# Optimization experiments

Measured on AMD Instinct MI355X. Metric: run time of the kernel, lower is better.

Reference implementation:

```python
import jax, jax.numpy as jnp
import numpy as np

B, T, D = 2, 2048, 2048
H, HD = 16, 128
HHD = HD // 2
SCALE = 1.0 / np.sqrt(HHD).astype(np.float32)


def setup_inputs() -> dict:
    key = jax.random.key(0)
    ks = jax.random.split(key, 6)
    s = 1.0 / np.sqrt(D).astype(np.float32)
    return {
        "x": jax.random.normal(ks[0], (B, T, D), jnp.float32),
        "Wq": jax.random.normal(ks[1], (D, H * HD), jnp.float32) * s,
        "Wk": jax.random.normal(ks[2], (D, H * HD), jnp.float32) * s,
        "Wv": jax.random.normal(ks[3], (D, H * HD), jnp.float32) * s,
        "Wo": jax.random.normal(ks[4], (H * HD, D), jnp.float32) * s,
        "lambda_init": jnp.full((H,), -0.2, jnp.float32),
    }


def reference(x, Wq, Wk, Wv, Wo, lambda_init):
    b, t, d = x.shape
    # projections -> (B, H, T, HD)
    q = (x @ Wq).reshape(b, t, H, HD).transpose(0, 2, 1, 3)
    k = (x @ Wk).reshape(b, t, H, HD).transpose(0, 2, 1, 3)
    v = (x @ Wv).reshape(b, t, H, HD).transpose(0, 2, 1, 3)
    q1, q2 = q[..., :HHD], q[..., HHD:]
    k1, k2 = k[..., :HHD], k[..., HHD:]
    scores1 = jnp.einsum('bhtc,bhsc->bhts', q1, k1) * SCALE
    scores2 = jnp.einsum('bhtc,bhsc->bhts', q2, k2) * SCALE
    causal = jnp.tril(jnp.ones((t, t), bool))  # (T, T)
    neg_inf = jnp.float32(-jnp.inf)
    scores1 = jnp.where(causal[None, None], scores1, neg_inf)
    scores2 = jnp.where(causal[None, None], scores2, neg_inf)
    attn1 = jax.nn.softmax(scores1, axis=-1)
    attn2 = jax.nn.softmax(scores2, axis=-1)
    lam = jax.nn.sigmoid(lambda_init)[None, :, None, None]
    diff_attn = attn1 - lam * attn2
    out = jnp.einsum('bhts,bhsd->bhtd', diff_attn, v)
    out = out.transpose(0, 2, 1, 3).reshape(b, t, H * HD)
    return out @ Wo
```

## Files before the change

kernel.cpp:

```cpp
#include <hip/hip_runtime.h>
#include <cstdint>
#include <cstddef>


typedef unsigned short u16;
typedef __bf16 bf16x8 __attribute__((ext_vector_type(8)));
typedef float f32x4 __attribute__((ext_vector_type(4)));

#define LOG2E 1.44269504088896340736f
#define KS 0.18033688011112042f
#define CB 11.541560327111707f

__device__ __forceinline__ u16 f2bu(float f) {
  unsigned int x = __float_as_uint(f);
  x += 0x7fffu + ((x >> 16) & 1u);
  return (u16)(x >> 16);
}

__device__ __forceinline__ void stage16(const void* g, void* lds_uniform, int lane) {
#if defined(__has_builtin) && __has_builtin(__builtin_amdgcn_global_load_lds)
  (void)lane;
  __builtin_amdgcn_global_load_lds(
      (__attribute__((address_space(1))) void*)(g),
      (__attribute__((address_space(3))) void*)(lds_uniform), 16, 0, 0);
#else
  *(uint4*)((char*)lds_uniform + lane * 16) = *(const uint4*)g;
#endif
}

__global__ void f32_to_bf16_k(const float* __restrict__ in, u16* __restrict__ out, int n4) {
  int i = blockIdx.x * blockDim.x + threadIdx.x;
  if (i < n4) {
    float4 v = ((const float4*)in)[i];
    ushort4 u;
    u.x = f2bu(v.x); u.y = f2bu(v.y); u.z = f2bu(v.z); u.w = f2bu(v.w);
    ((ushort4*)out)[i] = u;
  }
}

__global__ void transpose_f32_bf16(const float* __restrict__ in, u16* __restrict__ out,
                                   int R, int C) {
  __shared__ u16 tile[32][33];
  const int tx = threadIdx.x & 31, ty = threadIdx.x >> 5;
  const int c0 = blockIdx.x * 32, r0 = blockIdx.y * 32;
#pragma unroll
  for (int i = 0; i < 32; i += 8)
    tile[ty + i][tx] = f2bu(in[(size_t)(r0 + ty + i) * C + c0 + tx]);
  __syncthreads();
#pragma unroll
  for (int i = 0; i < 32; i += 8)
    out[(size_t)(c0 + ty + i) * R + r0 + tx] = tile[tx][ty + i];
}

template <int MODE>
__global__ void gemm_bt(const u16* __restrict__ A, const u16* __restrict__ BT,
                        void* __restrict__ C, u16* __restrict__ C2,
                        int Mdim, int Ndim, int Kdim) {
  __shared__ __align__(16) u16 As[128 * 32];
  __shared__ __align__(16) u16 Bs[128 * 32];
  const int tid = threadIdx.x;
  const int lane = tid & 63;
  const int w = tid >> 6;
  const int wm = w & 1, wn = w >> 1;
  const int li = lane & 15, lh = lane >> 4;
  const int m0 = blockIdx.x * 128;
  const int n0 = blockIdx.y * 128;

  const f32x4 fzero = {0.f, 0.f, 0.f, 0.f};
  f32x4 acc[4][4];
#pragma unroll
  for (int i = 0; i < 4; ++i)
#pragma unroll
    for (int jj = 0; jj < 4; ++jj) acc[i][jj] = fzero;

  for (int k0 = 0; k0 < Kdim; k0 += 32) {
#pragma unroll
    for (int i = 0; i < 2; ++i) {
      const int c = i * 256 + w * 64 + lane;
      stage16(A + (size_t)(m0 + (c >> 2)) * Kdim + k0 + ((c & 3) << 3),
              (char*)As + (size_t)(i * 256 + w * 64) * 16, lane);
      stage16(BT + (size_t)(n0 + (c >> 2)) * Kdim + k0 + ((c & 3) << 3),
              (char*)Bs + (size_t)(i * 256 + w * 64) * 16, lane);
    }
    __syncthreads();

    bf16x8 af[4], bfr[4];
#pragma unroll
    for (int mt = 0; mt < 4; ++mt)
      af[mt] = *(const bf16x8*)&As[(wm * 64 + mt * 16 + li) * 32 + lh * 8];
#pragma unroll
    for (int nt = 0; nt < 4; ++nt)
      bfr[nt] = *(const bf16x8*)&Bs[(wn * 64 + nt * 16 + li) * 32 + lh * 8];
#pragma unroll
    for (int mt = 0; mt < 4; ++mt)
#pragma unroll
      for (int nt = 0; nt < 4; ++nt)
        acc[mt][nt] = __builtin_amdgcn_mfma_f32_16x16x32_bf16(af[mt], bfr[nt], acc[mt][nt], 0, 0, 0);
    __syncthreads();
  }

#pragma unroll
  for (int mt = 0; mt < 4; ++mt) {
#pragma unroll
    for (int nt = 0; nt < 4; ++nt) {
      const int mb = m0 + wm * 64 + mt * 16 + lh * 4;
      const int n = n0 + wn * 64 + nt * 16 + li;
      if (MODE == 0) {
        u16* o = (u16*)C;
#pragma unroll
        for (int r = 0; r < 4; ++r)
          o[(size_t)(mb + r) * Ndim + n] = f2bu(acc[mt][nt][r]);
      } else if (MODE == 1) {
        float* o = (float*)C;
#pragma unroll
        for (int r = 0; r < 4; ++r)
          o[(size_t)(mb + r) * Ndim + n] = acc[mt][nt][r];
      } else {
        u16* o = (u16*)C;
        const int bb = mb >> 11, t = mb & 2047;
        const int hh = n >> 7, d = n & 127;
        ushort4 u;
        u.x = f2bu(acc[mt][nt][0]);
        u.y = f2bu(acc[mt][nt][1]);
        u.z = f2bu(acc[mt][nt][2]);
        u.w = f2bu(acc[mt][nt][3]);
        *(ushort4*)&o[((size_t)((bb * 16 + hh) * 128 + d) << 11) + t] = u;
      }
    }
  }
}

__device__ __forceinline__ void stage_half256(const u16* __restrict__ gbase, int Kdim,
                                              u16* lds_slot, int tid) {
#pragma unroll
  for (int j = 0; j < 2; ++j) {
    const int c = j * 512 + tid;
    const int ks = c >> 9;
    const int o = (c & 511) << 4;
    const int osz = o ^ (((o >> 9) & 1) << 5);
    const int row = osz >> 6;
    const int kel = (osz & 63) >> 1;
    stage16(gbase + (size_t)row * Kdim + ks * 32 + kel,
            (char*)lds_slot + ((size_t)(j * 512 + (tid & ~63)) << 4), tid & 63);
  }
}

#define PHASE256(MH, KS, LOADB, STAGESTMT, TAILSTMT)                           \
  {                                                                            \
    bf16x8 af[4];                                                              \
    _Pragma("unroll")                                                          \
    for (int mq = 0; mq < 4; ++mq)                                             \
      af[mq] = *(const bf16x8*)&As[sA][KS][((MH)*4 + mq) * 16 + li][lhx8];     \
    if (LOADB) {                                                               \
      _Pragma("unroll")                                                        \
      for (int nt = 0; nt < 4; ++nt)                                           \
        bfc[nt] = *(const bf16x8*)&Bs[sB][KS][brow + nt * 16 + li][lhx8];      \
    }                                                                          \
    STAGESTMT;                                                                 \
    __builtin_amdgcn_s_barrier();                                              \
    asm volatile("" ::: "memory");                                             \
    __builtin_amdgcn_s_setprio(1);                                             \
    _Pragma("unroll")                                                          \
    for (int mq = 0; mq < 4; ++mq) {                                           \
      _Pragma("unroll")                                                        \
      for (int nt = 0; nt < 4; ++nt)                                           \
        acc[(MH)*4 + mq][nt] = __builtin_amdgcn_mfma_f32_16x16x32_bf16(        \
            af[mq], bfc[nt], acc[(MH)*4 + mq][nt], 0, 0, 0);                   \
    }                                                                          \
    __builtin_amdgcn_s_setprio(0);                                             \
    TAILSTMT;                                                                  \
    __builtin_amdgcn_s_barrier();                                              \
    asm volatile("" ::: "memory");                                             \
  }

__global__ __launch_bounds__(512, 2)
void gemm256_qkv(const u16* __restrict__ A, const u16* __restrict__ BT,
                 u16* __restrict__ C, u16* __restrict__ C2, int Kdim) {
  __shared__ __align__(16) u16 As[5][2][128][32];
  __shared__ __align__(16) u16 Bs[4][2][128][32];

  const int tid = threadIdx.x;
  const int lane = tid & 63;
  const int w = tid >> 6;
  const int wm = w >> 2;
  const int wn = w & 3;
  const int li = lane & 15, lh = lane >> 4;
  const int lhx8 = (lh ^ (((li >> 3) & 1) << 1)) * 8;
  const int brow = (wn & 1) * 64;

  const int bid = blockIdx.x;
  const int xcd = bid & 7;
  const int local = bid >> 3;
  const int mtile = local / 3;
  const int ntile = xcd * 3 + (local % 3);
  const int m0 = mtile * 256, n0 = ntile * 256;

  const int NT = Kdim >> 6;
  const u16* Abase = A + (size_t)m0 * Kdim;
  const u16* Bbase = BT + (size_t)n0 * Kdim;

  auto stA = [&](int g) {
    if (g < 2 * NT)
      stage_half256(Abase + (size_t)((g & 1) * 128) * Kdim + (g >> 1) * 64, Kdim,
                    &As[g % 5][0][0][0], tid);
  };
  auto stB = [&](int g) {
    if (g < 2 * NT)
      stage_half256(Bbase + (size_t)((g & 1) * 128) * Kdim + (g >> 1) * 64, Kdim,
                    &Bs[g & 3][0][0][0], tid);
  };

  const f32x4 fzero = {0.f, 0.f, 0.f, 0.f};
  f32x4 acc[8][4];
#pragma unroll
  for (int i = 0; i < 8; ++i)
#pragma unroll
    for (int jj = 0; jj < 4; ++jj) acc[i][jj] = fzero;

  stA(0); stA(1); stB(0); stB(1); stA(2); stB(2); stB(3);
  asm volatile("s_waitcnt vmcnt(6)" ::: "memory");
  __builtin_amdgcn_s_barrier();
  asm volatile("" ::: "memory");

  bf16x8 bfc[4];
  for (int kt = 0; kt < NT; ++kt) {
    const int sA = (2 * kt + wm) % 5;
    const int sB = (2 * kt + (wn >> 1)) & 3;
    PHASE256(0, 0, 1, { stA(2 * kt + 3); stA(2 * kt + 4); }, ((void)0));
    PHASE256(1, 0, 0, ((void)0), ((void)0));
    PHASE256(0, 1, 1, ((void)0), ((void)0));
    PHASE256(1, 1, 0, { stB(2 * kt + 4); stB(2 * kt + 5); },
             if (kt + 2 < NT) { asm volatile("s_waitcnt vmcnt(6)" ::: "memory"); }
             else             { asm volatile("s_waitcnt vmcnt(0)" ::: "memory"); });
  }

  const int proj = n0 >> 11;
  const int nB = (n0 & 2047) + wn * 64;
  const int mB = m0 + wm * 128;
#pragma unroll
  for (int mt = 0; mt < 8; ++mt) {
#pragma unroll
    for (int nt = 0; nt < 4; ++nt) {
      const int mb = mB + mt * 16 + lh * 4;
      const int n = nB + nt * 16 + li;
      if (proj < 2) {
        u16* o = C + (size_t)proj * 4096 * 2048;
#pragma unroll
        for (int r = 0; r < 4; ++r)
          o[(size_t)(mb + r) * 2048 + n] = f2bu(acc[mt][nt][r]);
      } else {
        const int bb = mb >> 11, t = mb & 2047;
        const int hh = n >> 7, d = n & 127;
        ushort4 u;
        u.x = f2bu(acc[mt][nt][0]);
        u.y = f2bu(acc[mt][nt][1]);
        u.z = f2bu(acc[mt][nt][2]);
        u.w = f2bu(acc[mt][nt][3]);
        *(ushort4*)&C2[((size_t)((bb * 16 + hh) * 128 + d) << 11) + t] = u;
      }
    }
  }
}

__device__ __forceinline__ void stage_kv(const u16* __restrict__ kbase,
                                         const u16* __restrict__ vbase, int j,
                                         u16* ksBuf, u16* vsBuf, int w, int lane) {
  const int kst_r = lane >> 4, kst_c = lane & 15;
  const int vst_r = lane >> 3, vst_c = lane & 7;
#pragma unroll
  for (int i = 0; i < 4; ++i) {
    const int t = w * 4 + i;
    const int srow = t * 4 + kst_r;
    const int scb = kst_c ^ (srow & 7);
    stage16(kbase + (size_t)(j * 64 + srow) * 2048 + scb * 8,
            (char*)ksBuf + t * 1024, lane);
    const int drow = t * 8 + vst_r;
    const int dcb = vst_c ^ (drow & 7);
    stage16(vbase + (size_t)drow * 2048 + j * 64 + dcb * 8,
            (char*)vsBuf + t * 1024, lane);
  }
}

__global__ __launch_bounds__(256, 2)
void diff_attn(const u16* __restrict__ Q, const u16* __restrict__ K,
               const u16* __restrict__ VT, const float* __restrict__ lamin,
               u16* __restrict__ AO) {
  __shared__ __align__(16) u16 Ks[2][64 * 128];
  __shared__ __align__(16) u16 Vs[2][128 * 64];
  __shared__ __align__(16) u16 Ps1[64 * 64];
  __shared__ __align__(16) u16 Ps2[64 * 64];

  const int tid = threadIdx.x, lane = tid & 63, w = tid >> 6;
  const int li = lane & 15, lh = lane >> 4;
  const int bh = blockIdx.x & 31, pair = blockIdx.x >> 5;
  const int b = bh >> 4, h = bh & 15;

  const float lam = 1.f / (1.f + exp2f(-lamin[h] * LOG2E));
  const u16* kbase = K + ((size_t)(b * 2048)) * 2048 + h * 128;
  const u16* vbase = VT + ((size_t)(b * 16 + h) << 18);
  const f32x4 fzero = {0.f, 0.f, 0.f, 0.f};

  for (int phase = 0; phase < 2; ++phase) {
    const int it = phase ? 31 - pair : pair;
    const int t0 = it * 64;

    bf16x8 qf[4];
    {
      const u16* qp = Q + (size_t)(b * 2048 + t0 + w * 16 + li) * 2048 + h * 128 + lh * 8;
#pragma unroll
      for (int kk = 0; kk < 4; ++kk) qf[kk] = *(const bf16x8*)(qp + kk * 32);
    }

    f32x4 o1[8], o2[8];
#pragma unroll
    for (int i = 0; i < 8; ++i) { o1[i] = fzero; o2[i] = fzero; }
    float l1p[4] = {0.f, 0.f, 0.f, 0.f};
    float l2p[4] = {0.f, 0.f, 0.f, 0.f};

    if (phase) __syncthreads();
    stage_kv(kbase, vbase, 0, Ks[0], Vs[0], w, lane);

    for (int j = 0; j <= it; ++j) {
      const int cur = j & 1;
      __syncthreads();
      if (j < it)
        stage_kv(kbase, vbase, j + 1, Ks[cur ^ 1], Vs[cur ^ 1], w, lane);

      const u16* __restrict__ ks = Ks[cur];
      const u16* __restrict__ vs = Vs[cur];
      const bool diag = (j == it);

#pragma unroll
      for (int nt = 0; nt < 4; ++nt) {
        const int srow = nt * 16 + li;
        const int sw = li & 7;
        bf16x8 b0 = *(const bf16x8*)&ks[srow * 128 + ((0 + lh) ^ sw) * 8];
        bf16x8 b1 = *(const bf16x8*)&ks[srow * 128 + ((4 + lh) ^ sw) * 8];
        bf16x8 b2 = *(const bf16x8*)&ks[srow * 128 + ((8 + lh) ^ sw) * 8];
        bf16x8 b3 = *(const bf16x8*)&ks[srow * 128 + ((12 + lh) ^ sw) * 8];
        f32x4 s1 = fzero, s2 = fzero;
        s1 = __builtin_amdgcn_mfma_f32_16x16x32_bf16(qf[0], b0, s1, 0, 0, 0);
        s1 = __builtin_amdgcn_mfma_f32_16x16x32_bf16(qf[1], b1, s1, 0, 0, 0);
        s2 = __builtin_amdgcn_mfma_f32_16x16x32_bf16(qf[2], b2, s2, 0, 0, 0);
        s2 = __builtin_amdgcn_mfma_f32_16x16x32_bf16(qf[3], b3, s2, 0, 0, 0);

        const int cb = nt * 2 + (li >> 3);
        const int sg = j * 64 + nt * 16 + li;
#pragma unroll
        for (int r = 0; r < 4; ++r) {
          const int row = w * 16 + lh * 4 + r;
          float p1, p2;
          if (diag && sg > t0 + row) {
            p1 = 0.f; p2 = 0.f;
          } else {
            p1 = exp2f(fmaf(s1[r], KS, -CB));
            p2 = exp2f(fmaf(s2[r], KS, -CB));
          }
          l1p[r] += p1; l2p[r] += p2;
          const int idx = row * 64 + ((cb ^ (row & 7)) << 3) + (li & 7);
          Ps1[idx] = f2bu(p1);
          Ps2[idx] = f2bu(p2);
        }
      }

#pragma unroll
      for (int kss = 0; kss < 2; ++kss) {
        const int arow = w * 16 + li;
        const int jb = ((kss * 4 + lh) ^ (li & 7)) * 8;
        bf16x8 a1f = *(const bf16x8*)&Ps1[arow * 64 + jb];
        bf16x8 a2f = *(const bf16x8*)&Ps2[arow * 64 + jb];
#pragma unroll
        for (int nt = 0; nt < 8; ++nt) {
          const int d = nt * 16 + li;
          bf16x8 vf = *(const bf16x8*)&vs[d * 64 + ((kss * 4 + lh) ^ (li & 7)) * 8];
          o1[nt] = __builtin_amdgcn_mfma_f32_16x16x32_bf16(a1f, vf, o1[nt], 0, 0, 0);
          o2[nt] = __builtin_amdgcn_mfma_f32_16x16x32_bf16(a2f, vf, o2[nt], 0, 0, 0);
        }
      }
    }

#pragma unroll
    for (int r = 0; r < 4; ++r) {
#pragma unroll
      for (int off = 1; off < 16; off <<= 1) {
        l1p[r] += __shfl_xor(l1p[r], off);
        l2p[r] += __shfl_xor(l2p[r], off);
      }
    }

#pragma unroll
    for (int r = 0; r < 4; ++r) {
      const float inv1 = 1.f / l1p[r];
      const float inv2 = lam / l2p[r];
      u16* orow = AO + (size_t)(b * 2048 + t0 + w * 16 + lh * 4 + r) * 2048 + h * 128 + li;
#pragma unroll
      for (int nt = 0; nt < 8; ++nt)
        orow[nt * 16] = f2bu(o1[nt][r] * inv1 - o2[nt][r] * inv2);
    }
  }
}

extern "C" void kernel_launch(void* const* d_in, const int* in_sizes, int n_in,
                              void* d_out, int out_size, void* d_ws, size_t ws_size,
                              hipStream_t stream) {
  const float* x   = (const float*)d_in[0];
  const float* Wq  = (const float*)d_in[1];
  const float* Wk  = (const float*)d_in[2];
  const float* Wv  = (const float*)d_in[3];
  const float* Wo  = (const float*)d_in[4];
  const float* lam = (const float*)d_in[5];
  float* out = (float*)d_out;

  const size_t MB = 1ull << 20;
  char* ws = (char*)d_ws;
  u16* qb = (u16*)d_out;
  u16* kb = qb + (size_t)4096 * 2048;

  if (ws_size >= 56 * MB) {
    u16* xb = (u16*)(ws);
    u16* wT = (u16*)(ws + 16 * MB);
    u16* vt = (u16*)(ws + 40 * MB);
    u16* ao = xb;

    f32_to_bf16_k<<<8192, 256, 0, stream>>>(x, xb, 2097152);
    transpose_f32_bf16<<<dim3(64, 64), 256, 0, stream>>>(Wq, wT, 2048, 2048);
    transpose_f32_bf16<<<dim3(64, 64), 256, 0, stream>>>(Wk, wT + (size_t)4 * MB, 2048, 2048);
    transpose_f32_bf16<<<dim3(64, 64), 256, 0, stream>>>(Wv, wT + (size_t)8 * MB, 2048, 2048);
    gemm256_qkv<<<dim3(384), 512, 0, stream>>>(xb, wT, qb, vt, 2048);

    diff_attn<<<dim3(512), 256, 0, stream>>>(qb, kb, vt, lam, ao);

    transpose_f32_bf16<<<dim3(64, 64), 256, 0, stream>>>(Wo, wT, 2048, 2048);
    gemm_bt<1><<<dim3(32, 16), 256, 0, stream>>>(ao, wT, out, nullptr, 4096, 2048, 2048);
  } else {
    u16* xb = (u16*)(ws);
    u16* wT = (u16*)(ws + 16 * MB);
    u16* vt = (u16*)(ws + 24 * MB);
    u16* ao = xb;

    f32_to_bf16_k<<<8192, 256, 0, stream>>>(x, xb, 2097152);
    transpose_f32_bf16<<<dim3(64, 64), 256, 0, stream>>>(Wq, wT, 2048, 2048);
    gemm_bt<0><<<dim3(32, 16), 256, 0, stream>>>(xb, wT, qb, nullptr, 4096, 2048, 2048);
    transpose_f32_bf16<<<dim3(64, 64), 256, 0, stream>>>(Wk, wT, 2048, 2048);
    gemm_bt<0><<<dim3(32, 16), 256, 0, stream>>>(xb, wT, kb, nullptr, 4096, 2048, 2048);
    transpose_f32_bf16<<<dim3(64, 64), 256, 0, stream>>>(Wv, wT, 2048, 2048);
    gemm_bt<2><<<dim3(32, 16), 256, 0, stream>>>(xb, wT, vt, nullptr, 4096, 2048, 2048);

    diff_attn<<<dim3(512), 256, 0, stream>>>(qb, kb, vt, lam, ao);

    transpose_f32_bf16<<<dim3(64, 64), 256, 0, stream>>>(Wo, wT, 2048, 2048);
    gemm_bt<1><<<dim3(32, 16), 256, 0, stream>>>(ao, wT, out, nullptr, 4096, 2048, 2048);
  }
}
```

Baseline: 418.8 us.

## Restructure QKV GEMM staging into a 3-slot K=32 ring buffer pipeline

Rewrites the QKV projection GEMM mainloop to stage 256-row A and B tiles with K=32 per step into a three-slot LDS ring. It uses a hardcoded 4096-byte row stride, fixed trip counts and a simpler per-wave LDS addressing scheme. Each step has two phases, with one A or B stage issued per phase and a vmcnt wait of 4. This is meant to cut index arithmetic and barriers per unit of MFMA work. Occupancy drops to one block per CU via launch_bounds(512,1), and Kdim becomes a hardcoded constant.

```diff
diff --git a/kernel.cpp b/kernel.cpp
--- a/kernel.cpp
+++ b/kernel.cpp
@@ -25,6 +25,17 @@
       (__attribute__((address_space(3))) void*)(lds_uniform), 16, 0, 0);
 #else
   *(uint4*)((char*)lds_uniform + lane * 16) = *(const uint4*)g;
+#endif
+}
+
+__device__ __forceinline__ void stageK(const char* g, char* lds_u) {
+#if defined(__has_builtin) && __has_builtin(__builtin_amdgcn_global_load_lds)
+  __builtin_amdgcn_global_load_lds(
+      (__attribute__((address_space(1))) void*)g,
+      (__attribute__((address_space(3))) void*)lds_u, 16, 0, 0);
+  __builtin_amdgcn_global_load_lds(
+      (__attribute__((address_space(1))) void*)(g + (size_t)128 * 4096),
+      (__attribute__((address_space(3))) void*)(lds_u + 8192), 16, 0, 0);
 #endif
 }
 
@@ -130,33 +141,68 @@
   }
 }
 
-__device__ __forceinline__ void stage_half256(const u16* __restrict__ gbase, int Kdim,
-                                              u16* lds_slot, int tid) {
-#pragma unroll
-  for (int j = 0; j < 2; ++j) {
-    const int c = j * 512 + tid;
-    const int ks = c >> 9;
-    const int o = (c & 511) << 4;
-    const int osz = o ^ (((o >> 9) & 1) << 5);
-    const int row = osz >> 6;
-    const int kel = (osz & 63) >> 1;
-    stage16(gbase + (size_t)row * Kdim + ks * 32 + kel,
-            (char*)lds_slot + ((size_t)(j * 512 + (tid & ~63)) << 4), tid & 63);
-  }
-}
-
-#define PHASE256(MH, KS, LOADB, STAGESTMT, TAILSTMT)                           \
+__global__ __launch_bounds__(512, 1)
+void gemm256_qkv(const u16* __restrict__ A, const u16* __restrict__ BT,
+                 u16* __restrict__ C, u16* __restrict__ C2, int ) {
+  __shared__ __align__(16) u16 As[3][256][32];
+  __shared__ __align__(16) u16 Bs[3][256][32];
+
+  const int tid = threadIdx.x;
+  const int lane = tid & 63;
+  const int w = tid >> 6;
+  const int wm = w >> 2;
+  const int wn = w & 3;
+  const int li = lane & 15, lh = lane >> 4;
+  const int lhx8 = (lh ^ (((li >> 3) & 1) << 1)) * 8;
+
+  const int bid = blockIdx.x;
+  const int xcd = bid & 7;
+  const int local = bid >> 3;
+  const int mtile = local / 3;
+  const int ntile = xcd * 3 + (local % 3);
+  const int m0 = mtile * 256, n0 = ntile * 256;
+
+  const int srow = tid >> 2;
+  const int schk = (tid & 3) ^ (((tid >> 5) & 1) << 1);
+  const size_t soff = (size_t)srow * 4096 + (size_t)schk * 16;
+
+  const char* pA = (const char*)A  + (size_t)m0 * 4096 + soff;
+  const char* pB = (const char*)BT + (size_t)n0 * 4096 + soff;
+
+  const char* aB = (const char*)As + (size_t)(wm * 128 + li) * 64 + lhx8 * 2;
+  const char* bB = (const char*)Bs + (size_t)(wn * 64 + li) * 64 + lhx8 * 2;
+  char* const AsW = (char*)As + w * 1024;
+  char* const BsW = (char*)Bs + w * 1024;
+
+#define STAGE_A(SLOT) { stageK(pA, AsW + (SLOT) * 16384); pA += 64; }
+#define STAGE_B(SLOT) { stageK(pB, BsW + (SLOT) * 16384); pB += 64; }
+
+  const f32x4 fzero = {0.f, 0.f, 0.f, 0.f};
+  f32x4 acc[8][4];
+#pragma unroll
+  for (int i = 0; i < 8; ++i)
+#pragma unroll
+    for (int jj = 0; jj < 4; ++jj) acc[i][jj] = fzero;
+
+  STAGE_A(0); STAGE_B(0); STAGE_A(1); STAGE_B(1);
+  asm volatile("s_waitcnt vmcnt(4)" ::: "memory");
+  __builtin_amdgcn_s_barrier();
+  asm volatile("" ::: "memory");
+
+  bf16x8 bfc[4];
+
+#define QPH(SLOT, P, LOADB, STAGES, TAIL)                                      \
   {                                                                            \
     bf16x8 af[4];                                                              \
     _Pragma("unroll")                                                          \
     for (int mq = 0; mq < 4; ++mq)                                             \
-      af[mq] = *(const bf16x8*)&As[sA][KS][((MH)*4 + mq) * 16 + li][lhx8];     \
+      af[mq] = *(const bf16x8*)(aB + (SLOT) * 16384 + ((P) * 4 + mq) * 1024);  \
     if (LOADB) {                                                               \
       _Pragma("unroll")                                                        \
       for (int nt = 0; nt < 4; ++nt)                                           \
-        bfc[nt] = *(const bf16x8*)&Bs[sB][KS][brow + nt * 16 + li][lhx8];      \
+        bfc[nt] = *(const bf16x8*)(bB + (SLOT) * 16384 + nt * 1024);           \
     }                                                                          \
-    STAGESTMT;                                                                 \
+    STAGES;                                                                    \
     __builtin_amdgcn_s_barrier();                                              \
     asm volatile("" ::: "memory");                                             \
     __builtin_amdgcn_s_setprio(1);                                             \
@@ -164,75 +210,36 @@
     for (int mq = 0; mq < 4; ++mq) {                                           \
       _Pragma("unroll")                                                        \
       for (int nt = 0; nt < 4; ++nt)                                           \
-        acc[(MH)*4 + mq][nt] = __builtin_amdgcn_mfma_f32_16x16x32_bf16(        \
-            af[mq], bfc[nt], acc[(MH)*4 + mq][nt], 0, 0, 0);                   \
+        acc[(P) * 4 + mq][nt] = __builtin_amdgcn_mfma_f32_16x16x32_bf16(       \
+            af[mq], bfc[nt], acc[(P) * 4 + mq][nt], 0, 0, 0);                  \
     }                                                                          \
     __builtin_amdgcn_s_setprio(0);                                             \
-    TAILSTMT;                                                                  \
+    TAIL;                                                                      \
     __builtin_amdgcn_s_barrier();                                              \
     asm volatile("" ::: "memory");                                             \
   }
 
-__global__ __launch_bounds__(512, 2)
-void gemm256_qkv(const u16* __restrict__ A, const u16* __restrict__ BT,
-                 u16* __restrict__ C, u16* __restrict__ C2, int Kdim) {
-  __shared__ __align__(16) u16 As[5][2][128][32];
-  __shared__ __align__(16) u16 Bs[4][2][128][32];
-
-  const int tid = threadIdx.x;
-  const int lane = tid & 63;
-  const int w = tid >> 6;
-  const int wm = w >> 2;
-  const int wn = w & 3;
-  const int li = lane & 15, lh = lane >> 4;
-  const int lhx8 = (lh ^ (((li >> 3) & 1) << 1)) * 8;
-  const int brow = (wn & 1) * 64;
-
-  const int bid = blockIdx.x;
-  const int xcd = bid & 7;
-  const int local = bid >> 3;
-  const int mtile = local / 3;
-  const int ntile = xcd * 3 + (local % 3);
-  const int m0 = mtile * 256, n0 = ntile * 256;
-
-  const int NT = Kdim >> 6;
-  const u16* Abase = A + (size_t)m0 * Kdim;
-  const u16* Bbase = BT + (size_t)n0 * Kdim;
-
-  auto stA = [&](int g) {
-    if (g < 2 * NT)
-      stage_half256(Abase + (size_t)((g & 1) * 128) * Kdim + (g >> 1) * 64, Kdim,
-                    &As[g % 5][0][0][0], tid);
-  };
-  auto stB = [&](int g) {
-    if (g < 2 * NT)
-      stage_half256(Bbase + (size_t)((g & 1) * 128) * Kdim + (g >> 1) * 64, Kdim,
-                    &Bs[g & 3][0][0][0], tid);
-  };
-
-  const f32x4 fzero = {0.f, 0.f, 0.f, 0.f};
-  f32x4 acc[8][4];
-#pragma unroll
-  for (int i = 0; i < 8; ++i)
-#pragma unroll
-    for (int jj = 0; jj < 4; ++jj) acc[i][jj] = fzero;
-
-  stA(0); stA(1); stB(0); stB(1); stA(2); stB(2); stB(3);
-  asm volatile("s_waitcnt vmcnt(6)" ::: "memory");
-  __builtin_amdgcn_s_barrier();
-  asm volatile("" ::: "memory");
-
-  bf16x8 bfc[4];
-  for (int kt = 0; kt < NT; ++kt) {
-    const int sA = (2 * kt + wm) % 5;
-    const int sB = (2 * kt + (wn >> 1)) & 3;
-    PHASE256(0, 0, 1, { stA(2 * kt + 3); stA(2 * kt + 4); }, ((void)0));
-    PHASE256(1, 0, 0, ((void)0), ((void)0));
-    PHASE256(0, 1, 1, ((void)0), ((void)0));
-    PHASE256(1, 1, 0, { stB(2 * kt + 4); stB(2 * kt + 5); },
-             if (kt + 2 < NT) { asm volatile("s_waitcnt vmcnt(6)" ::: "memory"); }
-             else             { asm volatile("s_waitcnt vmcnt(0)" ::: "memory"); });
-  }
+#define KSTEP_MAIN(J3)                                                         \
+  QPH((J3), 0, 1, { STAGE_A(((J3) + 2) % 3); }, ((void)0))                     \
+  QPH((J3), 1, 0, { STAGE_B(((J3) + 2) % 3); },                                \
+      asm volatile("s_waitcnt vmcnt(4)" ::: "memory"))
+
+  for (int t3 = 0; t3 < 20; ++t3) {
+    KSTEP_MAIN(0)
+    KSTEP_MAIN(1)
+    KSTEP_MAIN(2)
+  }
+  KSTEP_MAIN(0)
+  KSTEP_MAIN(1)
+  QPH(2, 0, 1, ((void)0), ((void)0))
+  QPH(2, 1, 0, ((void)0), asm volatile("s_waitcnt vmcnt(0)" ::: "memory"))
+  QPH(0, 0, 1, ((void)0), ((void)0))
+  QPH(0, 1, 0, ((void)0), ((void)0))
+
+#undef QPH
+#undef KSTEP_MAIN
+#undef STAGE_A
+#undef STAGE_B
 
   const int proj = n0 >> 11;
   const int nB = (n0 & 2047) + wn * 64;
```

Result: no change. 415.5 us (-0.8%).
